# Kernel optimization log

Measured on AMD Instinct MI355X. Metric: run time of the kernel, lower is better.

Reference implementation:

```python
import jax, jax.numpy as jnp
import numpy as np

N = 100000
E = 1600000
IN_DIM = 128
HEADS = 4
OUT_DIM = 32


def setup_inputs() -> dict:
    key = jax.random.key(0)
    k1, k2, k3, k4, k5 = jax.random.split(key, 5)
    x = jax.random.normal(k1, (N, IN_DIM), dtype=jnp.float32)
    edge_index = jax.random.randint(k2, (2, E), 0, N, dtype=jnp.int64)
    # torch Linear weight: (out_features, in_features) = (HEADS*OUT_DIM, IN_DIM)
    W = jax.random.normal(k3, (HEADS * OUT_DIM, IN_DIM), dtype=jnp.float32) * 0.05
    a_src = jax.random.normal(k4, (HEADS, OUT_DIM), dtype=jnp.float32)
    a_dst = jax.random.normal(k5, (HEADS, OUT_DIM), dtype=jnp.float32)
    return {"x": x, "edge_index": edge_index, "W": W, "a_src": a_src, "a_dst": a_dst}


def reference(x, edge_index, W, a_src, a_dst):
    n = x.shape[0]
    H, D = a_src.shape
    # h: (N, H, D)
    h = (x @ W.T).reshape(n, H, D)
    src, dst = edge_index[0], edge_index[1]
    # per-edge attention logits: (E, H)
    e_src = jnp.einsum('ehd,hd->eh', h[src], a_src)
    e_dst = jnp.einsum('ehd,hd->eh', h[dst], a_dst)
    e = jax.nn.leaky_relu(e_src + e_dst, negative_slope=0.2)
    # segment max per destination node (init zeros, include_self=True as in torch)
    e_max = jnp.zeros((n, H), dtype=x.dtype).at[dst].max(e)
    e_exp = jnp.exp(e - e_max[dst])
    e_sum = jnp.zeros((n, H), dtype=x.dtype).at[dst].add(e_exp)
    alpha = e_exp / (e_sum[dst] + 1e-8)  # (E, H)
    # weighted messages and scatter-add aggregation
    msg = h[src] * alpha[..., None]  # (E, H, D)
    out = jnp.zeros((n, H, D), dtype=x.dtype).at[dst].add(msg)
    return out.reshape(n, H * D)  # concat=True
```

## Files before the change

### kernel.cpp

```cpp
#include <hip/hip_runtime.h>

#define IN_DIM 128
#define HD 128
#define HEADS 4
#define MD 64
#define CAP 128
#define NCOHORT 8

__device__ __forceinline__ float lrelu(float v){ return v > 0.f ? v : 0.2f*v; }
__device__ __forceinline__ float4 add4(float4 a, float4 b){
  return make_float4(a.x+b.x, a.y+b.y, a.z+b.z, a.w+b.w);
}
__device__ __forceinline__ float4 expl4(float4 v){
  return make_float4(__expf(lrelu(v.x)), __expf(lrelu(v.y)), __expf(lrelu(v.z)), __expf(lrelu(v.w)));
}
__device__ __forceinline__ unsigned short f2b(float f){
  unsigned u = __float_as_uint(f);
  return (unsigned short)((u + 0x7FFFu + ((u >> 16) & 1u)) >> 16);
}
__device__ __forceinline__ float b2f(unsigned short b){
  return __uint_as_float(((unsigned)b) << 16);
}
__device__ __forceinline__ float blo(unsigned u){ return __uint_as_float(u << 16); }
__device__ __forceinline__ float bhi(unsigned u){ return __uint_as_float(u & 0xFFFF0000u); }

__global__ __launch_bounds__(256) void k_init(const float* __restrict__ W, float* __restrict__ WT,
                                              int* __restrict__ count, int n_nodes){
  int idx = blockIdx.x*256 + threadIdx.x;
  if (idx < 128*128){ int j = idx >> 7, k = idx & 127; WT[k*128 + j] = W[idx]; }
  for (int n = idx; n < n_nodes; n += gridDim.x*256) count[n] = 0;
}

__global__ __launch_bounds__(256) void k_gemm_scatter(
    const float* __restrict__ x, const float* __restrict__ WT,
    const float* __restrict__ a_src, const float* __restrict__ a_dst,
    unsigned short* __restrict__ h, float* __restrict__ s, float* __restrict__ t,
    const int* __restrict__ esrc, const int* __restrict__ edst, int E_,
    int* __restrict__ count, int* __restrict__ slots,
    int n_nodes, int n_tiles, int n_tiles_pad, int sc_blocks, int R){
  __shared__ float xs[64][132];
  const int tid = threadIdx.x;

  if ((int)blockIdx.x < n_tiles){
    const int jg  = tid & 31;
    const int ng  = tid >> 5;
    const int j4  = jg*4;
    const float4 as4 = *(const float4*)(a_src + j4);
    const float4 ad4 = *(const float4*)(a_dst + j4);
    const int base = blockIdx.x*64;

    for (int i = tid; i < 64*32; i += 256){
      int row = i >> 5, c4 = (i & 31)*4;
      float4 v = make_float4(0.f,0.f,0.f,0.f);
      if (base + row < n_nodes) v = *(const float4*)(x + (size_t)(base+row)*IN_DIM + c4);
      *(float4*)&xs[row][c4] = v;
    }
    __syncthreads();

    float acc[8][4];
    #pragma unroll
    for (int i=0;i<8;++i){ acc[i][0]=acc[i][1]=acc[i][2]=acc[i][3]=0.f; }
    const int nb = ng*8;

    for (int k=0;k<128;k+=4){
      float4 w0 = *(const float4*)(WT + (k  )*128 + j4);
      float4 w1 = *(const float4*)(WT + (k+1)*128 + j4);
      float4 w2 = *(const float4*)(WT + (k+2)*128 + j4);
      float4 w3 = *(const float4*)(WT + (k+3)*128 + j4);
      #pragma unroll
      for (int i=0;i<8;++i){
        float4 xv = *(const float4*)&xs[nb+i][k];
        acc[i][0] = fmaf(w0.x, xv.x, acc[i][0]);
        acc[i][1] = fmaf(w0.y, xv.x, acc[i][1]);
        acc[i][2] = fmaf(w0.z, xv.x, acc[i][2]);
        acc[i][3] = fmaf(w0.w, xv.x, acc[i][3]);
        acc[i][0] = fmaf(w1.x, xv.y, acc[i][0]);
        acc[i][1] = fmaf(w1.y, xv.y, acc[i][1]);
        acc[i][2] = fmaf(w1.z, xv.y, acc[i][2]);
        acc[i][3] = fmaf(w1.w, xv.y, acc[i][3]);
        acc[i][0] = fmaf(w2.x, xv.z, acc[i][0]);
        acc[i][1] = fmaf(w2.y, xv.z, acc[i][1]);
        acc[i][2] = fmaf(w2.z, xv.z, acc[i][2]);
        acc[i][3] = fmaf(w2.w, xv.z, acc[i][3]);
        acc[i][0] = fmaf(w3.x, xv.w, acc[i][0]);
        acc[i][1] = fmaf(w3.y, xv.w, acc[i][1]);
        acc[i][2] = fmaf(w3.z, xv.w, acc[i][2]);
        acc[i][3] = fmaf(w3.w, xv.w, acc[i][3]);
      }
    }

    #pragma unroll
    for (int i=0;i<8;++i){
      int node = base + nb + i;
      if (node < n_nodes)
        *(ushort4*)(h + (size_t)node*HD + j4) =
          make_ushort4(f2b(acc[i][0]), f2b(acc[i][1]), f2b(acc[i][2]), f2b(acc[i][3]));
    }
    #pragma unroll
    for (int i=0;i<8;++i){
      float ps = acc[i][0]*as4.x + acc[i][1]*as4.y + acc[i][2]*as4.z + acc[i][3]*as4.w;
      float pt = acc[i][0]*ad4.x + acc[i][1]*ad4.y + acc[i][2]*ad4.z + acc[i][3]*ad4.w;
      ps += __shfl_xor(ps,1,64); ps += __shfl_xor(ps,2,64); ps += __shfl_xor(ps,4,64);
      pt += __shfl_xor(pt,1,64); pt += __shfl_xor(pt,2,64); pt += __shfl_xor(pt,4,64);
      if ((jg & 7) == 0){
        int node = base + nb + i;
        if (node < n_nodes){
          int hh = jg >> 3;
          s[node*HEADS + hh] = ps;
          t[node*HEADS + hh] = pt;
        }
      }
    }
  } else if ((int)blockIdx.x >= n_tiles_pad){
    const int sb = blockIdx.x - n_tiles_pad;
    const unsigned c = blockIdx.x & (NCOHORT-1);
    const int g  = (sb >> 3)*256 + tid;
    const int gs = (sc_blocks >> 3)*256;
    const unsigned lo = c*(unsigned)R;
    for (int e = g; e < E_; e += gs){
      unsigned d = (unsigned)edst[e];
      if (d - lo < (unsigned)R){
        int pos = atomicAdd(&count[d], 1);
        if (pos < MD) slots[(size_t)d*MD + pos] = esrc[e];
      }
    }
  }
}

__global__ __launch_bounds__(256) void k_aggregate2(const int* __restrict__ slots,
    const int* __restrict__ count, const unsigned short* __restrict__ h,
    const float* __restrict__ s, const float* __restrict__ t,
    float* __restrict__ out, int n_nodes){
  __shared__ int   s_src[4][MD];
  __shared__ float s_exp[4][MD][4];
  const int lane = threadIdx.x & 63;
  const int slot = threadIdx.x >> 6;
  const int n = blockIdx.x*4 + slot;
  if (n >= n_nodes) return;
  int cnt = count[n]; if (cnt > MD) cnt = MD;
  const float4 t4 = *(const float4*)(t + n*HEADS);

  float4 z4 = make_float4(0.f,0.f,0.f,0.f);
  if (lane < cnt){
    int src = slots[(size_t)n*MD + lane];
    s_src[slot][lane] = src;
    float4 s4 = *(const float4*)(s + src*HEADS);
    float4 e4 = expl4(add4(s4, t4));
    z4 = e4;
    *(float4*)&s_exp[slot][lane][0] = e4;
  }
  #pragma unroll
  for (int o=1;o<64;o<<=1){
    z4.x += __shfl_xor(z4.x,o,64);
    z4.y += __shfl_xor(z4.y,o,64);
    z4.z += __shfl_xor(z4.z,o,64);
    z4.w += __shfl_xor(z4.w,o,64);
  }

  const int qtr = lane >> 4;
  const int q   = lane & 15;
  const int hd  = q >> 2;
  float zh = hd==0 ? z4.x : hd==1 ? z4.y : hd==2 ? z4.z : z4.w;
  const float r = 1.f/(zh + 1e-8f);
  float4 accA = make_float4(0.f,0.f,0.f,0.f);
  float4 accB = make_float4(0.f,0.f,0.f,0.f);
  const unsigned short* hq = h + 8*q;

#define FMA8(U, W) \
  accA.x = fmaf(W, blo(U.x), accA.x); accA.y = fmaf(W, bhi(U.x), accA.y); \
  accA.z = fmaf(W, blo(U.y), accA.z); accA.w = fmaf(W, bhi(U.y), accA.w); \
  accB.x = fmaf(W, blo(U.z), accB.x); accB.y = fmaf(W, bhi(U.z), accB.y); \
  accB.z = fmaf(W, blo(U.w), accB.z); accB.w = fmaf(W, bhi(U.w), accB.w);

  int i = 0;
  for (; i + 8 <= cnt; i += 8){
    int eA = i + qtr, eB = i + 4 + qtr;
    int aA = s_src[slot][eA], aB = s_src[slot][eB];
    uint4 uA = *(const uint4*)(hq + (size_t)aA*HD);
    uint4 uB = *(const uint4*)(hq + (size_t)aB*HD);
    float wA = s_exp[slot][eA][hd], wB = s_exp[slot][eB][hd];
    FMA8(uA, wA); FMA8(uB, wB);
  }
  if (i + 4 <= cnt){
    int eA = i + qtr;
    int aA = s_src[slot][eA];
    uint4 uA = *(const uint4*)(hq + (size_t)aA*HD);
    float wA = s_exp[slot][eA][hd];
    FMA8(uA, wA);
    i += 4;
  }
  if (i < cnt && qtr < cnt - i){
    int eA = i + qtr;
    int aA = s_src[slot][eA];
    uint4 uA = *(const uint4*)(hq + (size_t)aA*HD);
    float wA = s_exp[slot][eA][hd];
    FMA8(uA, wA);
  }
#undef FMA8

  #pragma unroll
  for (int o=16;o<64;o<<=1){
    accA.x += __shfl_xor(accA.x,o,64); accA.y += __shfl_xor(accA.y,o,64);
    accA.z += __shfl_xor(accA.z,o,64); accA.w += __shfl_xor(accA.w,o,64);
    accB.x += __shfl_xor(accB.x,o,64); accB.y += __shfl_xor(accB.y,o,64);
    accB.z += __shfl_xor(accB.z,o,64); accB.w += __shfl_xor(accB.w,o,64);
  }
  if (qtr == 0){
    *(float4*)(out + (size_t)n*HD + 8*q)     = make_float4(accA.x*r, accA.y*r, accA.z*r, accA.w*r);
    *(float4*)(out + (size_t)n*HD + 8*q + 4) = make_float4(accB.x*r, accB.y*r, accB.z*r, accB.w*r);
  }
}

__global__ __launch_bounds__(256) void k_transpose_w(const float* __restrict__ W, float* __restrict__ WT){
  int idx = blockIdx.x*256 + threadIdx.x;
  int j = idx >> 7, k = idx & 127;
  WT[k*128 + j] = W[idx];
}

__global__ __launch_bounds__(256) void k_gemm(const float* __restrict__ x, const float* __restrict__ WT,
    const float* __restrict__ a_src, const float* __restrict__ a_dst,
    unsigned short* __restrict__ h, float* __restrict__ s, float* __restrict__ t,
    int n_nodes, int n_tiles){
  __shared__ float xs[64][132];
  const int tid = threadIdx.x;
  const int jg  = tid & 31;
  const int ng  = tid >> 5;
  const int j4  = jg*4;
  const float4 as4 = *(const float4*)(a_src + j4);
  const float4 ad4 = *(const float4*)(a_dst + j4);

  for (int tile = blockIdx.x; tile < n_tiles; tile += gridDim.x){
    const int base = tile*64;
    __syncthreads();
    for (int i = tid; i < 64*32; i += 256){
      int row = i >> 5, c4 = (i & 31)*4;
      float4 v = make_float4(0.f,0.f,0.f,0.f);
      if (base + row < n_nodes) v = *(const float4*)(x + (size_t)(base+row)*IN_DIM + c4);
      *(float4*)&xs[row][c4] = v;
    }
    __syncthreads();

    float acc[8][4];
    #pragma unroll
    for (int i=0;i<8;++i){ acc[i][0]=acc[i][1]=acc[i][2]=acc[i][3]=0.f; }
    const int nb = ng*8;
    for (int k=0;k<128;k+=4){
      float4 w0 = *(const float4*)(WT + (k  )*128 + j4);
      float4 w1 = *(const float4*)(WT + (k+1)*128 + j4);
      float4 w2 = *(const float4*)(WT + (k+2)*128 + j4);
      float4 w3 = *(const float4*)(WT + (k+3)*128 + j4);
      #pragma unroll
      for (int i=0;i<8;++i){
        float4 xv = *(const float4*)&xs[nb+i][k];
        acc[i][0] = fmaf(w0.x, xv.x, acc[i][0]); acc[i][1] = fmaf(w0.y, xv.x, acc[i][1]);
        acc[i][2] = fmaf(w0.z, xv.x, acc[i][2]); acc[i][3] = fmaf(w0.w, xv.x, acc[i][3]);
        acc[i][0] = fmaf(w1.x, xv.y, acc[i][0]); acc[i][1] = fmaf(w1.y, xv.y, acc[i][1]);
        acc[i][2] = fmaf(w1.z, xv.y, acc[i][2]); acc[i][3] = fmaf(w1.w, xv.y, acc[i][3]);
        acc[i][0] = fmaf(w2.x, xv.z, acc[i][0]); acc[i][1] = fmaf(w2.y, xv.z, acc[i][1]);
        acc[i][2] = fmaf(w2.z, xv.z, acc[i][2]); acc[i][3] = fmaf(w2.w, xv.z, acc[i][3]);
        acc[i][0] = fmaf(w3.x, xv.w, acc[i][0]); acc[i][1] = fmaf(w3.y, xv.w, acc[i][1]);
        acc[i][2] = fmaf(w3.z, xv.w, acc[i][2]); acc[i][3] = fmaf(w3.w, xv.w, acc[i][3]);
      }
    }
    #pragma unroll
    for (int i=0;i<8;++i){
      int node = base + nb + i;
      if (node < n_nodes)
        *(ushort4*)(h + (size_t)node*HD + j4) =
          make_ushort4(f2b(acc[i][0]), f2b(acc[i][1]), f2b(acc[i][2]), f2b(acc[i][3]));
    }
    #pragma unroll
    for (int i=0;i<8;++i){
      float ps = acc[i][0]*as4.x + acc[i][1]*as4.y + acc[i][2]*as4.z + acc[i][3]*as4.w;
      float pt = acc[i][0]*ad4.x + acc[i][1]*ad4.y + acc[i][2]*ad4.z + acc[i][3]*ad4.w;
      ps += __shfl_xor(ps,1,64); ps += __shfl_xor(ps,2,64); ps += __shfl_xor(ps,4,64);
      pt += __shfl_xor(pt,1,64); pt += __shfl_xor(pt,2,64); pt += __shfl_xor(pt,4,64);
      if ((jg & 7) == 0){
        int node = base + nb + i;
        if (node < n_nodes){
          int hh = jg >> 3;
          s[node*HEADS + hh] = ps;
          t[node*HEADS + hh] = pt;
        }
      }
    }
  }
}

__global__ __launch_bounds__(256) void k_hist(const int* __restrict__ dst, int E_,
                                              int* __restrict__ count, int R){
  const int c  = blockIdx.x & (NCOHORT-1);
  const int g  = (blockIdx.x >> 3)*256 + threadIdx.x;
  const int gs = (gridDim.x >> 3)*256;
  const unsigned lo = (unsigned)(c*R);
  for (int e = g; e < E_; e += gs){
    unsigned d = (unsigned)dst[e];
    if (d - lo < (unsigned)R) atomicAdd(&count[d], 1);
  }
}

__global__ void k_offsets(const int* __restrict__ count, int n_nodes,
                          int* __restrict__ offs, int* __restrict__ wcur, int* __restrict__ cursor){
  int n = blockIdx.x*blockDim.x + threadIdx.x;
  int lane = threadIdx.x & 63;
  int c = (n < n_nodes) ? count[n] : 0;
  int incl = c;
  #pragma unroll
  for (int o=1;o<64;o<<=1){
    int v = __shfl_up(incl, o, 64);
    if (lane >= o) incl += v;
  }
  int wave_total = __shfl(incl, 63, 64);
  int base = 0;
  if (lane == 63) base = atomicAdd(cursor, wave_total);
  base = __shfl(base, 63, 64);
  if (n < n_nodes){
    int off = base + incl - c;
    offs[n] = off; wcur[n] = off;
  }
}

__global__ __launch_bounds__(256) void k_scatter(const int* __restrict__ src, const int* __restrict__ dst,
                                                 int E_, int* __restrict__ wcur,
                                                 int* __restrict__ csr_src, int R){
  const int c  = blockIdx.x & (NCOHORT-1);
  const int g  = (blockIdx.x >> 3)*256 + threadIdx.x;
  const int gs = (gridDim.x >> 3)*256;
  const unsigned lo = (unsigned)(c*R);
  for (int e = g; e < E_; e += gs){
    unsigned d = (unsigned)dst[e];
    if (d - lo < (unsigned)R){
      int pos = atomicAdd(&wcur[d], 1);
      csr_src[pos] = src[e];
    }
  }
}

__global__ __launch_bounds__(256) void k_aggregate(const int* __restrict__ csr_src,
    const int* __restrict__ offs, const int* __restrict__ count,
    const unsigned short* __restrict__ h, const float* __restrict__ s, const float* __restrict__ t,
    float* __restrict__ out, int n_nodes){
  __shared__ int   s_src[4][CAP];
  __shared__ float s_exp[4][CAP][4];
  const int lane = threadIdx.x & 63;
  const int slot = threadIdx.x >> 6;
  const int n = blockIdx.x*4 + slot;
  if (n >= n_nodes) return;
  const int start = offs[n];
  const int cnt   = count[n];
  const float4 t4 = *(const float4*)(t + n*HEADS);
  const bool fast = (cnt <= CAP);

  float4 z4 = make_float4(0.f,0.f,0.f,0.f);
  if (fast){
    #pragma unroll
    for (int j=0;j<2;++j){
      int i = lane + j*64;
      if (i < cnt){
        int src = csr_src[start+i];
        s_src[slot][i] = src;
        float4 s4 = *(const float4*)(s + src*HEADS);
        float4 e4 = expl4(add4(s4, t4));
        z4 = add4(z4, e4);
        *(float4*)&s_exp[slot][i][0] = e4;
      }
    }
  } else {
    for (int i = lane; i < cnt; i += 64){
      int src = csr_src[start+i];
      float4 s4 = *(const float4*)(s + src*HEADS);
      z4 = add4(z4, expl4(add4(s4, t4)));
    }
  }
  #pragma unroll
  for (int o=1;o<64;o<<=1){
    z4.x += __shfl_xor(z4.x,o,64);
    z4.y += __shfl_xor(z4.y,o,64);
    z4.z += __shfl_xor(z4.z,o,64);
    z4.w += __shfl_xor(z4.w,o,64);
  }

  if (fast){
    const int half = lane >> 5;
    const int fl   = lane & 31;
    const int hd   = fl >> 3;
    float zh = hd==0 ? z4.x : hd==1 ? z4.y : hd==2 ? z4.z : z4.w;
    const float r = 1.f/(zh + 1e-8f);
    float4 acc = make_float4(0.f,0.f,0.f,0.f);
    int i = 0;
    for (; i + 4 <= cnt; i += 4){
      int a0 = s_src[slot][i+half], a1 = s_src[slot][i+2+half];
      ushort4 u0 = *(const ushort4*)(h + (size_t)a0*HD + 4*fl);
      ushort4 u1 = *(const ushort4*)(h + (size_t)a1*HD + 4*fl);
      float e0 = s_exp[slot][i+half][hd], e1 = s_exp[slot][i+2+half][hd];
      acc.x = fmaf(e0, b2f(u0.x), acc.x); acc.y = fmaf(e0, b2f(u0.y), acc.y);
      acc.z = fmaf(e0, b2f(u0.z), acc.z); acc.w = fmaf(e0, b2f(u0.w), acc.w);
      acc.x = fmaf(e1, b2f(u1.x), acc.x); acc.y = fmaf(e1, b2f(u1.y), acc.y);
      acc.z = fmaf(e1, b2f(u1.z), acc.z); acc.w = fmaf(e1, b2f(u1.w), acc.w);
    }
    if (i + 2 <= cnt){
      int a0 = s_src[slot][i+half];
      ushort4 u0 = *(const ushort4*)(h + (size_t)a0*HD + 4*fl);
      float e0 = s_exp[slot][i+half][hd];
      acc.x = fmaf(e0, b2f(u0.x), acc.x); acc.y = fmaf(e0, b2f(u0.y), acc.y);
      acc.z = fmaf(e0, b2f(u0.z), acc.z); acc.w = fmaf(e0, b2f(u0.w), acc.w);
      i += 2;
    }
    if (i < cnt && half == 0){
      int a0 = s_src[slot][i];
      ushort4 u0 = *(const ushort4*)(h + (size_t)a0*HD + 4*fl);
      float e0 = s_exp[slot][i][hd];
      acc.x = fmaf(e0, b2f(u0.x), acc.x); acc.y = fmaf(e0, b2f(u0.y), acc.y);
      acc.z = fmaf(e0, b2f(u0.z), acc.z); acc.w = fmaf(e0, b2f(u0.w), acc.w);
    }
    acc.x += __shfl_xor(acc.x, 32, 64);
    acc.y += __shfl_xor(acc.y, 32, 64);
    acc.z += __shfl_xor(acc.z, 32, 64);
    acc.w += __shfl_xor(acc.w, 32, 64);
    if (half == 0){
      *(float4*)(out + (size_t)n*HD + 4*fl) = make_float4(acc.x*r, acc.y*r, acc.z*r, acc.w*r);
    }
  } else {
    const int hd = lane >> 4;
    float zh = hd==0 ? z4.x : hd==1 ? z4.y : hd==2 ? z4.z : z4.w;
    const float r = 1.f/(zh + 1e-8f);
    float th = hd==0 ? t4.x : hd==1 ? t4.y : hd==2 ? t4.z : t4.w;
    float2 acc = make_float2(0.f,0.f);
    for (int i = 0; i < cnt; ++i){
      int src = csr_src[start+i];
      float4 s4 = *(const float4*)(s + src*HEADS);
      float sh = hd==0 ? s4.x : hd==1 ? s4.y : hd==2 ? s4.z : s4.w;
      float e = __expf(lrelu(sh+th));
      ushort2 u = *(const ushort2*)(h + (size_t)src*HD + 2*lane);
      acc.x = fmaf(e, b2f(u.x), acc.x); acc.y = fmaf(e, b2f(u.y), acc.y);
    }
    *(float2*)(out + (size_t)n*HD + 2*lane) = make_float2(acc.x*r, acc.y*r);
  }
}

extern "C" void kernel_launch(void* const* d_in, const int* in_sizes, int n_in,
                              void* d_out, int out_size, void* d_ws, size_t ws_size,
                              hipStream_t stream) {
  const float* x     = (const float*)d_in[0];
  const int*   ei    = (const int*)d_in[1];
  const float* W     = (const float*)d_in[2];
  const float* a_src = (const float*)d_in[3];
  const float* a_dst = (const float*)d_in[4];
  float* out = (float*)d_out;

  const int n_nodes = in_sizes[0] / IN_DIM;
  const int E_      = in_sizes[1] / 2;
  const int R       = (n_nodes + NCOHORT - 1) / NCOHORT;

  char* ws = (char*)d_ws;
  size_t off = 0;
  auto alloc = [&](size_t bytes){ size_t cur = off; off += (bytes + 255) & ~255ULL; return cur; };

  float*          WT    = (float*)(ws + alloc(128*128*4));
  unsigned short* h     = (unsigned short*)(ws + alloc((size_t)n_nodes*HD*2));
  float*          s     = (float*)(ws + alloc((size_t)n_nodes*HEADS*4));
  float*          t     = (float*)(ws + alloc((size_t)n_nodes*HEADS*4));
  int*            count = (int*)  (ws + alloc((size_t)n_nodes*4));

  size_t slotted_need = off + (((size_t)n_nodes*MD*4 + 255) & ~255ULL);

  const int n_tiles = (n_nodes + 63) / 64;

  if (ws_size >= slotted_need){
    int* slots = (int*)(ws + alloc((size_t)n_nodes*MD*4));

    int init_grid = (n_nodes + 255)/256; if (init_grid < 64) init_grid = 64;
    k_init<<<init_grid, 256, 0, stream>>>(W, WT, count, n_nodes);

    const int n_tiles_pad = (n_tiles + 7) & ~7;
    const int sc_blocks   = 2048;
    k_gemm_scatter<<<n_tiles_pad + sc_blocks, 256, 0, stream>>>(
        x, WT, a_src, a_dst, h, s, t, ei, ei + E_, E_,
        count, slots, n_nodes, n_tiles, n_tiles_pad, sc_blocks, R);

    k_aggregate2<<<(n_nodes+3)/4, 256, 0, stream>>>(slots, count, h, s, t, out, n_nodes);
  } else {
    int* offs    = (int*)(ws + alloc((size_t)n_nodes*4));
    int* wcur    = (int*)(ws + alloc((size_t)n_nodes*4));
    int* cursor  = (int*)(ws + alloc(4));
    int* csr_src = (int*)(ws + alloc((size_t)E_*4));

    hipMemsetAsync(count, 0, (size_t)n_nodes*4, stream);
    hipMemsetAsync(cursor, 0, 4, stream);
    k_transpose_w<<<64, 256, 0, stream>>>(W, WT);
    k_gemm<<<n_tiles, 256, 0, stream>>>(x, WT, a_src, a_dst, h, s, t, n_nodes, n_tiles);
    k_hist<<<2048, 256, 0, stream>>>(ei + E_, E_, count, R);
    k_offsets<<<(n_nodes+255)/256, 256, 0, stream>>>(count, n_nodes, offs, wcur, cursor);
    k_scatter<<<2048, 256, 0, stream>>>(ei, ei + E_, E_, wcur, csr_src, R);
    k_aggregate<<<(n_nodes+3)/4, 256, 0, stream>>>(csr_src, offs, count, h, s, t, out, n_nodes);
  }
}
```

Baseline: 203.1 us.

## Interleave GEMM tiles and scatter blocks in fused grid; prefetch W rows

Block indices are regrouped so that every fourth group of 8 blocks runs the edge-scatter work and the other three groups run GEMM tiles. Scatter then executes concurrently with the GEMM instead of trailing it at the end of the grid, and the scatter block count now scales with the number of tiles rather than being fixed at 2048. The GEMM inner loop also loads the next four W rows into registers one step ahead, hiding global load latency. This costs extra registers, and the smaller scatter grid may lower throughput for the atomic slotting.

```diff
diff --git a/kernel.cpp b/kernel.cpp
--- a/kernel.cpp
+++ b/kernel.cpp
@@ -37,17 +37,23 @@
     unsigned short* __restrict__ h, float* __restrict__ s, float* __restrict__ t,
     const int* __restrict__ esrc, const int* __restrict__ edst, int E_,
     int* __restrict__ count, int* __restrict__ slots,
-    int n_nodes, int n_tiles, int n_tiles_pad, int sc_blocks, int R){
+    int n_nodes, int n_tiles, int S, int R){
   __shared__ float xs[64][132];
-  const int tid = threadIdx.x;
-
-  if ((int)blockIdx.x < n_tiles){
+  const int tid   = threadIdx.x;
+  const int g     = blockIdx.x >> 3;
+  const int lane8 = blockIdx.x & 7;
+
+  if ((g & 3) != 3){
+    const int gg   = g - (g >> 2);
+    const int tile = gg*8 + lane8;
+    if (tile >= n_tiles) return;
+    const int base = tile*64;
+
     const int jg  = tid & 31;
     const int ng  = tid >> 5;
     const int j4  = jg*4;
     const float4 as4 = *(const float4*)(a_src + j4);
     const float4 ad4 = *(const float4*)(a_dst + j4);
-    const int base = blockIdx.x*64;
 
     for (int i = tid; i < 64*32; i += 256){
       int row = i >> 5, c4 = (i & 31)*4;
@@ -61,32 +67,39 @@
     #pragma unroll
     for (int i=0;i<8;++i){ acc[i][0]=acc[i][1]=acc[i][2]=acc[i][3]=0.f; }
     const int nb = ng*8;
-
+    const float* wp = WT + j4;
+
+    float4 wc0 = *(const float4*)(wp);
+    float4 wc1 = *(const float4*)(wp + 128);
+    float4 wc2 = *(const float4*)(wp + 256);
+    float4 wc3 = *(const float4*)(wp + 384);
     for (int k=0;k<128;k+=4){
-      float4 w0 = *(const float4*)(WT + (k  )*128 + j4);
-      float4 w1 = *(const float4*)(WT + (k+1)*128 + j4);
-      float4 w2 = *(const float4*)(WT + (k+2)*128 + j4);
-      float4 w3 = *(const float4*)(WT + (k+3)*128 + j4);
+      const float* wq = wp + (size_t)(((k+4) & 127))*128;
+      float4 wn0 = *(const float4*)(wq);
+      float4 wn1 = *(const float4*)(wq + 128);
+      float4 wn2 = *(const float4*)(wq + 256);
+      float4 wn3 = *(const float4*)(wq + 384);
       #pragma unroll
-      for (int i=0;i<8;++i){
-        float4 xv = *(const float4*)&xs[nb+i][k];
-        acc[i][0] = fmaf(w0.x, xv.x, acc[i][0]);
-        acc[i][1] = fmaf(w0.y, xv.x, acc[i][1]);
-        acc[i][2] = fmaf(w0.z, xv.x, acc[i][2]);
-        acc[i][3] = fmaf(w0.w, xv.x, acc[i][3]);
-        acc[i][0] = fmaf(w1.x, xv.y, acc[i][0]);
-        acc[i][1] = fmaf(w1.y, xv.y, acc[i][1]);
-        acc[i][2] = fmaf(w1.z, xv.y, acc[i][2]);
-        acc[i][3] = fmaf(w1.w, xv.y, acc[i][3]);
-        acc[i][0] = fmaf(w2.x, xv.z, acc[i][0]);
-        acc[i][1] = fmaf(w2.y, xv.z, acc[i][1]);
-        acc[i][2] = fmaf(w2.z, xv.z, acc[i][2]);
-        acc[i][3] = fmaf(w2.w, xv.z, acc[i][3]);
-        acc[i][0] = fmaf(w3.x, xv.w, acc[i][0]);
-        acc[i][1] = fmaf(w3.y, xv.w, acc[i][1]);
-        acc[i][2] = fmaf(w3.z, xv.w, acc[i][2]);
-        acc[i][3] = fmaf(w3.w, xv.w, acc[i][3]);
+      for (int u=0;u<8;++u){
+        float4 xv = *(const float4*)&xs[nb+u][k];
+        acc[u][0] = fmaf(wc0.x, xv.x, acc[u][0]);
+        acc[u][1] = fmaf(wc0.y, xv.x, acc[u][1]);
+        acc[u][2] = fmaf(wc0.z, xv.x, acc[u][2]);
+        acc[u][3] = fmaf(wc0.w, xv.x, acc[u][3]);
+        acc[u][0] = fmaf(wc1.x, xv.y, acc[u][0]);
+        acc[u][1] = fmaf(wc1.y, xv.y, acc[u][1]);
+        acc[u][2] = fmaf(wc1.z, xv.y, acc[u][2]);
+        acc[u][3] = fmaf(wc1.w, xv.y, acc[u][3]);
+        acc[u][0] = fmaf(wc2.x, xv.z, acc[u][0]);
+        acc[u][1] = fmaf(wc2.y, xv.z, acc[u][1]);
+        acc[u][2] = fmaf(wc2.z, xv.z, acc[u][2]);
+        acc[u][3] = fmaf(wc2.w, xv.z, acc[u][3]);
+        acc[u][0] = fmaf(wc3.x, xv.w, acc[u][0]);
+        acc[u][1] = fmaf(wc3.y, xv.w, acc[u][1]);
+        acc[u][2] = fmaf(wc3.z, xv.w, acc[u][2]);
+        acc[u][3] = fmaf(wc3.w, xv.w, acc[u][3]);
       }
+      wc0 = wn0; wc1 = wn1; wc2 = wn2; wc3 = wn3;
     }
 
     #pragma unroll
@@ -111,13 +124,12 @@
         }
       }
     }
-  } else if ((int)blockIdx.x >= n_tiles_pad){
-    const int sb = blockIdx.x - n_tiles_pad;
-    const unsigned c = blockIdx.x & (NCOHORT-1);
-    const int g  = (sb >> 3)*256 + tid;
-    const int gs = (sc_blocks >> 3)*256;
-    const unsigned lo = c*(unsigned)R;
-    for (int e = g; e < E_; e += gs){
+  } else {
+    const int m   = g >> 2;
+    const unsigned lo = (unsigned)(lane8 * R);
+    const int gth = m*256 + tid;
+    const int gstride = S*256;
+    for (int e = gth; e < E_; e += gstride){
       unsigned d = (unsigned)edst[e];
       if (d - lo < (unsigned)R){
         int pos = atomicAdd(&count[d], 1);
@@ -472,11 +484,12 @@
     int init_grid = (n_nodes + 255)/256; if (init_grid < 64) init_grid = 64;
     k_init<<<init_grid, 256, 0, stream>>>(W, WT, count, n_nodes);
 
-    const int n_tiles_pad = (n_tiles + 7) & ~7;
-    const int sc_blocks   = 2048;
-    k_gemm_scatter<<<n_tiles_pad + sc_blocks, 256, 0, stream>>>(
+    const int ngg = (n_tiles + 7) / 8;
+    int G = ( (ngg*4 + 2) / 3 + 3 ) & ~3;
+    const int S = G >> 2;
+    k_gemm_scatter<<<G*8, 256, 0, stream>>>(
         x, WT, a_src, a_dst, h, s, t, ei, ei + E_, E_,
-        count, slots, n_nodes, n_tiles, n_tiles_pad, sc_blocks, R);
+        count, slots, n_nodes, n_tiles, S, R);
 
     k_aggregate2<<<(n_nodes+3)/4, 256, 0, stream>>>(slots, count, h, s, t, out, n_nodes);
   } else {
```

Result: slower. 363.1 us (+78.8%).
